# Performance work log

Measured on AMD Instinct MI355X. Metric: run time of the kernel, lower is better.

## Reference

```python
import jax, jax.numpy as jnp
import numpy as np

NUM_NODES = 100000
NODE_FEAT_DIM = 512
EDGE_FEAT_DIM = 512
MEM_DIM = NODE_FEAT_DIM + EDGE_FEAT_DIM  # 1024
BATCH = 65536


def setup_inputs() -> dict:
    key = jax.random.key(0)
    k_ids, k_mem, k_emb, kq, ks, kk = jax.random.split(key, 6)
    scale = 1.0 / np.sqrt(MEM_DIM)
    inp = {
        "node_ids": jax.random.randint(k_ids, (BATCH,), 0, NUM_NODES, dtype=jnp.int64)
        if jax.config.jax_enable_x64 else
        jax.random.randint(k_ids, (BATCH,), 0, NUM_NODES, dtype=jnp.int32),
        # memory bank: (N, 1, D); randomized (instead of the zero init) so math is non-trivial
        "node_memories": jax.random.normal(k_mem, (NUM_NODES, 1, MEM_DIM), dtype=jnp.float32) * 0.02,
        "node_embedding": jax.random.normal(k_emb, (NUM_NODES, MEM_DIM), dtype=jnp.float32) * 0.02,
        "Wq": jax.random.normal(jax.random.fold_in(kq, 0), (MEM_DIM, NODE_FEAT_DIM), dtype=jnp.float32) * scale,
        "bq": jnp.zeros((NODE_FEAT_DIM,), dtype=jnp.float32),
        "Ws": jax.random.normal(jax.random.fold_in(ks, 0), (MEM_DIM, NODE_FEAT_DIM), dtype=jnp.float32) * scale,
        "bs": jnp.zeros((NODE_FEAT_DIM,), dtype=jnp.float32),
        "Wk": jax.random.normal(jax.random.fold_in(kk, 0), (MEM_DIM, NODE_FEAT_DIM), dtype=jnp.float32) * scale,
        "bk": jnp.zeros((NODE_FEAT_DIM,), dtype=jnp.float32),
    }
    return inp


def reference(node_ids, node_memories, node_embedding, Wq, bq, Ws, bs, Wk, bk):
    ids = node_ids.astype(jnp.int32)
    # torch.sum(node_memories[ids], dim=2): reduces feature dim -> (B, 1)
    mem_sum = jnp.sum(node_memories[ids], axis=2)          # (B, 1)
    x = mem_sum + node_embedding[ids]                      # broadcast -> (B, D)
    q = jax.nn.sigmoid(x @ Wq + bq)                        # (B, node_feat_dim)
    s = jax.nn.sigmoid(x @ Ws + bs)
    k = jax.nn.sigmoid(x @ Wk + bk)
    return (q, s, k)
```

## Files before the change

kernel.cpp:

```cpp
#include <hip/hip_runtime.h>
#include <hip/hip_bf16.h>
#include <stdint.h>

#define BATCH_N 65536
#define KDIM 1024
#define NTOT 1536

typedef __bf16 bf16x8 __attribute__((ext_vector_type(8)));
typedef float f32x4 __attribute__((ext_vector_type(4)));

__device__ __forceinline__ unsigned short f2bf(float f) {
    unsigned u = __builtin_bit_cast(unsigned, f);
    u += 0x7FFFu + ((u >> 16) & 1u);
    return (unsigned short)(u >> 16);
}

__global__ __launch_bounds__(256) void prep_kernel(
    const int* __restrict__ ids,
    const float* __restrict__ mem,
    const float* __restrict__ emb,
    unsigned short* __restrict__ x)
{
    const int b    = blockIdx.x * 4 + (threadIdx.x >> 6);
    const int lane = threadIdx.x & 63;
    const int id   = ids[b];
    const float4* m4 = (const float4*)(mem + (size_t)id * KDIM) + lane;
    const float4* e4 = (const float4*)(emb + (size_t)id * KDIM) + lane;
    float4 v0 = m4[0];
    float4 v1 = m4[64];
    float4 v2 = m4[128];
    float4 v3 = m4[192];
    float s = (v0.x + v0.y + v0.z + v0.w) + (v1.x + v1.y + v1.z + v1.w)
            + (v2.x + v2.y + v2.z + v2.w) + (v3.x + v3.y + v3.z + v3.w);
    #pragma unroll
    for (int off = 1; off < 64; off <<= 1) s += __shfl_xor(s, off, 64);
    unsigned short* xb = x + (size_t)b * KDIM;
    #pragma unroll
    for (int q = 0; q < 4; ++q) {
        float4 e = e4[q * 64];
        ushort4 o;
        o.x = f2bf(s + e.x);
        o.y = f2bf(s + e.y);
        o.z = f2bf(s + e.z);
        o.w = f2bf(s + e.w);
        const int k   = q * 256 + lane * 4;
        const int ksw = k ^ ((b & 7) << 3);
        *(ushort4*)(xb + ksw) = o;
    }
}

__global__ __launch_bounds__(256) void wconv_kernel(
    const float* __restrict__ Wq, const float* __restrict__ Ws,
    const float* __restrict__ Wk, unsigned short* __restrict__ wt)
{
    const int gt = blockIdx.x * 256 + threadIdx.x;
    const int n  = gt % NTOT;
    const int kb = (gt / NTOT) * 4;
    const float* W = (n < 512) ? Wq : ((n < 1024) ? Ws : Wk);
    const int nn = n & 511;
    ushort4 o;
    o.x = f2bf(W[(size_t)(kb + 0) * 512 + nn]);
    o.y = f2bf(W[(size_t)(kb + 1) * 512 + nn]);
    o.z = f2bf(W[(size_t)(kb + 2) * 512 + nn]);
    o.w = f2bf(W[(size_t)(kb + 3) * 512 + nn]);
    const int ksw = kb ^ ((n & 7) << 3);
    *(ushort4*)(wt + (size_t)n * KDIM + ksw) = o;
}

#define BM 256
#define BN 256
#define BK 64
#define MT (BATCH_N / BM)
#define NT (NTOT / BN)
#define NWG (MT * NT)

#define BAR() asm volatile("s_barrier" ::: "memory")
#define VM4() asm volatile("s_waitcnt vmcnt(4)" ::: "memory")
#define VM0() asm volatile("s_waitcnt vmcnt(0)" ::: "memory")
#define AS1 __attribute__((address_space(1)))
#define AS3 __attribute__((address_space(3)))

__global__ __launch_bounds__(512, 2) void gemm_kernel(
    const unsigned short* __restrict__ X,
    const unsigned short* __restrict__ Wt,
    const float* __restrict__ bq, const float* __restrict__ bs,
    const float* __restrict__ bk, float* __restrict__ out)
{
    __shared__ __align__(16) unsigned short sA[32768];
    __shared__ __align__(16) unsigned short sB[32768];

    const int tid  = threadIdx.x;
    const int xcd  = blockIdx.x & 7;
    const int idx  = blockIdx.x >> 3;
    const int wgid = xcd * (NWG / 8) + idx;
    const int nt   = wgid % NT;
    const int mt   = wgid / NT;
    const int m0   = mt * BM;
    const int n0   = nt * BN;
    const int wid  = tid >> 6;
    const int lane = tid & 63;
    const int wm   = wid >> 2;
    const int wn   = wid & 3;
    const int r16  = lane & 15;
    const int kb0  = (lane >> 4) << 4;
    const int ksw  = (r16 & 7) << 4;

    f32x4 acc[8][4];
    #pragma unroll
    for (int i = 0; i < 8; i++)
        #pragma unroll
        for (int j = 0; j < 4; j++)
            acc[i][j] = f32x4{0.f, 0.f, 0.f, 0.f};

    bf16x8 af0[4][2], af1[4][2], bfr0[2][2], bfr1[2][2];

    const unsigned short* gA = X  + (size_t)(m0 + (tid >> 3)) * KDIM + (tid & 7) * 8;
    const unsigned short* gB = Wt + (size_t)(n0 + (tid >> 3)) * KDIM + (tid & 7) * 8;
    const int ldst = (tid & 448) * 8;

#define STG_A(slot, h, kt) do {                                                 \
    _Pragma("unroll")                                                            \
    for (int c = 0; c < 2; ++c)                                                  \
        __builtin_amdgcn_global_load_lds(                                        \
            (const AS1 void*)(gA + (size_t)((h) * 128 + c * 64) * KDIM + (kt) * BK), \
            (AS3 void*)(&sA[((slot) * 2 + (h)) * 8192 + c * 4096 + ldst]),       \
            16, 0, 0);                                                           \
} while (0)
#define STG_B(slot, h, kt) do {                                                 \
    _Pragma("unroll")                                                            \
    for (int c = 0; c < 2; ++c)                                                  \
        __builtin_amdgcn_global_load_lds(                                        \
            (const AS1 void*)(gB + (size_t)((h) * 128 + c * 64) * KDIM + (kt) * BK), \
            (AS3 void*)(&sB[((slot) * 2 + (h)) * 8192 + c * 4096 + ldst]),       \
            16, 0, 0);                                                           \
} while (0)

#define LDA(SET, slot, qa) do {                                                 \
    const char* p = (const char*)&sA[((slot) * 2 + (qa)) * 8192];                \
    _Pragma("unroll")                                                            \
    for (int i = 0; i < 4; ++i)                                                  \
        _Pragma("unroll")                                                        \
        for (int kk = 0; kk < 2; ++kk)                                           \
            SET[i][kk] = *(const bf16x8*)(p + (wm * 64 + i * 16 + r16) * 128     \
                                            + ((kk * 64 + kb0) ^ ksw));          \
} while (0)
#define LDB(SET, slot, qb) do {                                                 \
    const char* p = (const char*)&sB[((slot) * 2 + (qb)) * 8192];                \
    _Pragma("unroll")                                                            \
    for (int j = 0; j < 2; ++j)                                                  \
        _Pragma("unroll")                                                        \
        for (int kk = 0; kk < 2; ++kk)                                           \
            SET[j][kk] = *(const bf16x8*)(p + (wn * 32 + j * 16 + r16) * 128     \
                                            + ((kk * 64 + kb0) ^ ksw));          \
} while (0)

#define MM(QA, QB, ASET, BSET) do {                                             \
    __builtin_amdgcn_s_setprio(1);                                               \
    _Pragma("unroll")                                                            \
    for (int i = 0; i < 4; ++i)                                                  \
        _Pragma("unroll")                                                        \
        for (int j = 0; j < 2; ++j)                                              \
            _Pragma("unroll")                                                    \
            for (int kk = 0; kk < 2; ++kk)                                       \
                acc[(QA) * 4 + i][(QB) * 2 + j] =                                \
                    __builtin_amdgcn_mfma_f32_16x16x32_bf16(                     \
                        ASET[i][kk], BSET[j][kk],                                \
                        acc[(QA) * 4 + i][(QB) * 2 + j], 0, 0, 0);               \
    __builtin_amdgcn_s_setprio(0);                                               \
} while (0)

    STG_A(0, 0, 0); STG_A(0, 1, 0); STG_B(0, 0, 0); STG_B(0, 1, 0);
    STG_A(1, 0, 1); STG_B(1, 1, 1); STG_A(1, 1, 1);
    VM0();
    BAR();
    LDA(af0, 0, 0); LDB(bfr0, 0, 0);

    #pragma unroll 1
    for (int t = 0; t < 7; ++t) {
        const int ka = 2 * t + 1, kb2 = 2 * t + 2, kc = 2 * t + 3;
        MM(0, 0, af0, bfr0);
        LDB(bfr1, 0, 1); STG_B(1, 0, ka);                        BAR();
        MM(0, 1, af0, bfr1);
        LDA(af1, 0, 1); STG_A(0, 0, kb2);                        BAR();
        MM(1, 1, af1, bfr1); STG_B(0, 1, kb2); VM4();            BAR();
        MM(1, 0, af1, bfr0);
        LDA(af0, 1, 0); LDB(bfr0, 1, 0); STG_A(0, 1, kb2);       BAR();
        MM(0, 0, af0, bfr0);
        LDB(bfr1, 1, 1); STG_B(0, 0, kb2);                       BAR();
        MM(0, 1, af0, bfr1);
        LDA(af1, 1, 1); STG_A(1, 0, kc);                         BAR();
        MM(1, 1, af1, bfr1); STG_B(1, 1, kc); VM4();             BAR();
        MM(1, 0, af1, bfr0);
        LDA(af0, 0, 0); LDB(bfr0, 0, 0); STG_A(1, 1, kc);        BAR();
    }
    MM(0, 0, af0, bfr0);
    LDB(bfr1, 0, 1); STG_B(1, 0, 15);                            BAR();
    MM(0, 1, af0, bfr1); LDA(af1, 0, 1);                         BAR();
    MM(1, 1, af1, bfr1); VM0();                                  BAR();
    MM(1, 0, af1, bfr0); LDA(af0, 1, 0); LDB(bfr0, 1, 0);        BAR();
    MM(0, 0, af0, bfr0); LDB(bfr1, 1, 1);                        BAR();
    MM(0, 1, af0, bfr1); LDA(af1, 1, 1);                         BAR();
    MM(1, 1, af1, bfr1);                                         BAR();
    MM(1, 0, af1, bfr0);

    const int grp = nt >> 1;
    const float* bias = (grp == 0) ? bq : ((grp == 1) ? bs : bk);
    float* obase = out + (size_t)grp * ((size_t)BATCH_N * 512);
    const int cb = (nt & 1) * 256;
    #pragma unroll
    for (int qb = 0; qb < 2; ++qb)
        #pragma unroll
        for (int j = 0; j < 2; ++j) {
            const int col = cb + qb * 128 + wn * 32 + j * 16 + r16;
            const float bv = bias[col];
            #pragma unroll
            for (int qa = 0; qa < 2; ++qa)
                #pragma unroll
                for (int i = 0; i < 4; ++i) {
                    const int rbase = m0 + qa * 128 + wm * 64 + i * 16 + ((lane >> 4) << 2);
                    #pragma unroll
                    for (int r = 0; r < 4; ++r) {
                        float v = acc[qa * 4 + i][qb * 2 + j][r] + bv;
                        v = 1.0f / (1.0f + __expf(-v));
                        __builtin_nontemporal_store(v, &obase[(size_t)(rbase + r) * 512 + col]);
                    }
                }
        }
#undef STG_A
#undef STG_B
#undef LDA
#undef LDB
#undef MM
}

extern "C" void kernel_launch(void* const* d_in, const int* in_sizes, int n_in,
                              void* d_out, int out_size, void* d_ws, size_t ws_size,
                              hipStream_t stream) {
    const int*   ids = (const int*)d_in[0];
    const float* mem = (const float*)d_in[1];
    const float* emb = (const float*)d_in[2];
    const float* Wq  = (const float*)d_in[3];
    const float* bq  = (const float*)d_in[4];
    const float* Ws  = (const float*)d_in[5];
    const float* bs  = (const float*)d_in[6];
    const float* Wk  = (const float*)d_in[7];
    const float* bk  = (const float*)d_in[8];
    float* out = (float*)d_out;

    unsigned short* x  = (unsigned short*)d_ws;
    unsigned short* wt = x + (size_t)BATCH_N * KDIM;

    hipLaunchKernelGGL(wconv_kernel, dim3(NTOT), dim3(256), 0, stream, Wq, Ws, Wk, wt);
    hipLaunchKernelGGL(prep_kernel, dim3(BATCH_N / 4), dim3(256), 0, stream, ids, mem, emb, x);
    hipLaunchKernelGGL(gemm_kernel, dim3(NWG), dim3(512), 0, stream,
                       x, wt, bq, bs, bk, out);
}
```

Baseline: 394.6 us.

## Switch GEMM to FP8 MFMA and fold memory-sum term via weight column sums

```diff
diff --git a/kernel.cpp b/kernel.cpp
--- a/kernel.cpp
+++ b/kernel.cpp
@@ -6,88 +6,101 @@
 #define KDIM 1024
 #define NTOT 1536
 
-typedef __bf16 bf16x8 __attribute__((ext_vector_type(8)));
+typedef long long i64;
 typedef float f32x4 __attribute__((ext_vector_type(4)));
 
-__device__ __forceinline__ unsigned short f2bf(float f) {
-    unsigned u = __builtin_bit_cast(unsigned, f);
-    u += 0x7FFFu + ((u >> 16) & 1u);
-    return (unsigned short)(u >> 16);
+__device__ __forceinline__ unsigned pk4(float4 f, float s) {
+    int w = __builtin_amdgcn_cvt_pk_fp8_f32(f.x * s, f.y * s, 0, false);
+    w = __builtin_amdgcn_cvt_pk_fp8_f32(f.z * s, f.w * s, w, true);
+    return (unsigned)w;
 }
 
 __global__ __launch_bounds__(256) void prep_kernel(
     const int* __restrict__ ids,
     const float* __restrict__ mem,
     const float* __restrict__ emb,
-    unsigned short* __restrict__ x)
+    unsigned char* __restrict__ x,
+    float* __restrict__ rs)
 {
     const int b    = blockIdx.x * 4 + (threadIdx.x >> 6);
     const int lane = threadIdx.x & 63;
     const int id   = ids[b];
     const float4* m4 = (const float4*)(mem + (size_t)id * KDIM) + lane;
-    const float4* e4 = (const float4*)(emb + (size_t)id * KDIM) + lane;
-    float4 v0 = m4[0];
-    float4 v1 = m4[64];
-    float4 v2 = m4[128];
-    float4 v3 = m4[192];
+    float4 v0 = m4[0], v1 = m4[64], v2 = m4[128], v3 = m4[192];
     float s = (v0.x + v0.y + v0.z + v0.w) + (v1.x + v1.y + v1.z + v1.w)
             + (v2.x + v2.y + v2.z + v2.w) + (v3.x + v3.y + v3.z + v3.w);
     #pragma unroll
     for (int off = 1; off < 64; off <<= 1) s += __shfl_xor(s, off, 64);
-    unsigned short* xb = x + (size_t)b * KDIM;
-    #pragma unroll
-    for (int q = 0; q < 4; ++q) {
-        float4 e = e4[q * 64];
-        ushort4 o;
-        o.x = f2bf(s + e.x);
-        o.y = f2bf(s + e.y);
-        o.z = f2bf(s + e.z);
-        o.w = f2bf(s + e.w);
-        const int k   = q * 256 + lane * 4;
-        const int ksw = k ^ ((b & 7) << 3);
-        *(ushort4*)(xb + ksw) = o;
-    }
+    if (lane == 0) rs[b] = s;
+
+    const float4* e4 = (const float4*)(emb + (size_t)id * KDIM) + lane * 4;
+    float4 f0 = e4[0], f1 = e4[1], f2 = e4[2], f3 = e4[3];
+    const unsigned w0 = pk4(f0, 64.f), w1 = pk4(f1, 64.f);
+    const unsigned w2 = pk4(f2, 64.f), w3 = pk4(f3, 64.f);
+    uint4 val = (b & 1) ? uint4{w2, w3, w0, w1} : uint4{w0, w1, w2, w3};
+    const int dst = (lane * 16) ^ (((b >> 1) & 3) << 4);
+    *(uint4*)(x + (size_t)b * KDIM + dst) = val;
 }
 
 __global__ __launch_bounds__(256) void wconv_kernel(
     const float* __restrict__ Wq, const float* __restrict__ Ws,
-    const float* __restrict__ Wk, unsigned short* __restrict__ wt)
-{
-    const int gt = blockIdx.x * 256 + threadIdx.x;
-    const int n  = gt % NTOT;
-    const int kb = (gt / NTOT) * 4;
+    const float* __restrict__ Wk, unsigned char* __restrict__ wt)
+{
+    const int gt  = blockIdx.x * 256 + threadIdx.x;
+    const int n   = gt % NTOT;
+    const int kb4 = (gt / NTOT) * 4;
     const float* W = (n < 512) ? Wq : ((n < 1024) ? Ws : Wk);
     const int nn = n & 511;
-    ushort4 o;
-    o.x = f2bf(W[(size_t)(kb + 0) * 512 + nn]);
-    o.y = f2bf(W[(size_t)(kb + 1) * 512 + nn]);
-    o.z = f2bf(W[(size_t)(kb + 2) * 512 + nn]);
-    o.w = f2bf(W[(size_t)(kb + 3) * 512 + nn]);
-    const int ksw = kb ^ ((n & 7) << 3);
-    *(ushort4*)(wt + (size_t)n * KDIM + ksw) = o;
+    float4 f;
+    f.x = W[(size_t)(kb4 + 0) * 512 + nn];
+    f.y = W[(size_t)(kb4 + 1) * 512 + nn];
+    f.z = W[(size_t)(kb4 + 2) * 512 + nn];
+    f.w = W[(size_t)(kb4 + 3) * 512 + nn];
+    const unsigned w = pk4(f, 64.f);
+    const int dst = kb4 ^ ((n & 7) << 3);
+    *(unsigned*)(wt + (size_t)n * KDIM + dst) = w;
+}
+
+__global__ __launch_bounds__(256) void colsum_kernel(
+    const float* __restrict__ Wq, const float* __restrict__ Ws,
+    const float* __restrict__ Wk, float* __restrict__ csum)
+{
+    const int gt = blockIdx.x * 256 + threadIdx.x;
+    const float* W = (gt < 512) ? Wq : ((gt < 1024) ? Ws : Wk);
+    const int n = gt & 511;
+    float s0 = 0.f, s1 = 0.f, s2 = 0.f, s3 = 0.f;
+    #pragma unroll 4
+    for (int k = 0; k < 1024; k += 4) {
+        s0 += W[(size_t)(k + 0) * 512 + n];
+        s1 += W[(size_t)(k + 1) * 512 + n];
+        s2 += W[(size_t)(k + 2) * 512 + n];
+        s3 += W[(size_t)(k + 3) * 512 + n];
+    }
+    csum[gt] = (s0 + s1) + (s2 + s3);
 }
 
 #define BM 256
 #define BN 256
-#define BK 64
 #define MT (BATCH_N / BM)
 #define NT (NTOT / BN)
 #define NWG (MT * NT)
 
 #define BAR() asm volatile("s_barrier" ::: "memory")
-#define VM4() asm volatile("s_waitcnt vmcnt(4)" ::: "memory")
+#define VM2() asm volatile("s_waitcnt vmcnt(2)" ::: "memory")
 #define VM0() asm volatile("s_waitcnt vmcnt(0)" ::: "memory")
 #define AS1 __attribute__((address_space(1)))
 #define AS3 __attribute__((address_space(3)))
 
 __global__ __launch_bounds__(512, 2) void gemm_kernel(
-    const unsigned short* __restrict__ X,
-    const unsigned short* __restrict__ Wt,
+    const unsigned char* __restrict__ X,
+    const unsigned char* __restrict__ Wt,
+    const float* __restrict__ csum,
+    const float* __restrict__ rs,
     const float* __restrict__ bq, const float* __restrict__ bs,
     const float* __restrict__ bk, float* __restrict__ out)
 {
-    __shared__ __align__(16) unsigned short sA[32768];
-    __shared__ __align__(16) unsigned short sB[32768];
+    __shared__ __align__(16) unsigned char sA[32768];
+    __shared__ __align__(16) unsigned char sB[32768];
 
     const int tid  = threadIdx.x;
     const int xcd  = blockIdx.x & 7;
@@ -102,8 +115,8 @@
     const int wm   = wid >> 2;
     const int wn   = wid & 3;
     const int r16  = lane & 15;
-    const int kb0  = (lane >> 4) << 4;
-    const int ksw  = (r16 & 7) << 4;
+    const int kb0  = (lane >> 4) << 3;
+    const int ksw  = (r16 & 7) << 3;
 
     f32x4 acc[8][4];
     #pragma unroll
@@ -112,28 +125,20 @@
         for (int j = 0; j < 4; j++)
             acc[i][j] = f32x4{0.f, 0.f, 0.f, 0.f};
 
-    bf16x8 af0[4][2], af1[4][2], bfr0[2][2], bfr1[2][2];
-
-    const unsigned short* gA = X  + (size_t)(m0 + (tid >> 3)) * KDIM + (tid & 7) * 8;
-    const unsigned short* gB = Wt + (size_t)(n0 + (tid >> 3)) * KDIM + (tid & 7) * 8;
-    const int ldst = (tid & 448) * 8;
-
-#define STG_A(slot, h, kt) do {                                                 \
-    _Pragma("unroll")                                                            \
-    for (int c = 0; c < 2; ++c)                                                  \
-        __builtin_amdgcn_global_load_lds(                                        \
-            (const AS1 void*)(gA + (size_t)((h) * 128 + c * 64) * KDIM + (kt) * BK), \
-            (AS3 void*)(&sA[((slot) * 2 + (h)) * 8192 + c * 4096 + ldst]),       \
-            16, 0, 0);                                                           \
-} while (0)
-#define STG_B(slot, h, kt) do {                                                 \
-    _Pragma("unroll")                                                            \
-    for (int c = 0; c < 2; ++c)                                                  \
-        __builtin_amdgcn_global_load_lds(                                        \
-            (const AS1 void*)(gB + (size_t)((h) * 128 + c * 64) * KDIM + (kt) * BK), \
-            (AS3 void*)(&sB[((slot) * 2 + (h)) * 8192 + c * 4096 + ldst]),       \
-            16, 0, 0);                                                           \
-} while (0)
+    i64 af0[4][2], af1[4][2], bfr0[2][2], bfr1[2][2];
+
+    const unsigned char* gA = X  + (size_t)(m0 + (tid >> 2)) * KDIM + (tid & 3) * 16;
+    const unsigned char* gB = Wt + (size_t)(n0 + (tid >> 2)) * KDIM + (tid & 3) * 16;
+    const int ldst = tid * 16;
+
+#define STG_A(slot, h, kt) \
+    __builtin_amdgcn_global_load_lds( \
+        (const AS1 void*)(gA + (size_t)(h) * 128 * KDIM + (kt) * 64), \
+        (AS3 void*)(&sA[((slot) * 2 + (h)) * 8192 + ldst]), 16, 0, 0)
+#define STG_B(slot, h, kt) \
+    __builtin_amdgcn_global_load_lds( \
+        (const AS1 void*)(gB + (size_t)(h) * 128 * KDIM + (kt) * 64), \
+        (AS3 void*)(&sB[((slot) * 2 + (h)) * 8192 + ldst]), 16, 0, 0)
 
 #define LDA(SET, slot, qa) do {                                                 \
     const char* p = (const char*)&sA[((slot) * 2 + (qa)) * 8192];                \
@@ -141,8 +146,8 @@
     for (int i = 0; i < 4; ++i)                                                  \
         _Pragma("unroll")                                                        \
         for (int kk = 0; kk < 2; ++kk)                                           \
-            SET[i][kk] = *(const bf16x8*)(p + (wm * 64 + i * 16 + r16) * 128     \
-                                            + ((kk * 64 + kb0) ^ ksw));          \
+            SET[i][kk] = *(const i64*)(p + (wm * 64 + i * 16 + r16) * 64         \
+                                         + ((kk * 32 + kb0) ^ ksw));             \
 } while (0)
 #define LDB(SET, slot, qb) do {                                                 \
     const char* p = (const char*)&sB[((slot) * 2 + (qb)) * 8192];                \
@@ -150,8 +155,8 @@
     for (int j = 0; j < 2; ++j)                                                  \
         _Pragma("unroll")                                                        \
         for (int kk = 0; kk < 2; ++kk)                                           \
-            SET[j][kk] = *(const bf16x8*)(p + (wn * 32 + j * 16 + r16) * 128     \
-                                            + ((kk * 64 + kb0) ^ ksw));          \
+            SET[j][kk] = *(const i64*)(p + (wn * 32 + j * 16 + r16) * 64         \
+                                         + ((kk * 32 + kb0) ^ ksw));             \
 } while (0)
 
 #define MM(QA, QB, ASET, BSET) do {                                             \
@@ -163,7 +168,7 @@
             _Pragma("unroll")                                                    \
             for (int kk = 0; kk < 2; ++kk)                                       \
                 acc[(QA) * 4 + i][(QB) * 2 + j] =                                \
-                    __builtin_amdgcn_mfma_f32_16x16x32_bf16(                     \
+                    __builtin_amdgcn_mfma_f32_16x16x32_fp8_fp8(                  \
                         ASET[i][kk], BSET[j][kk],                                \
                         acc[(QA) * 4 + i][(QB) * 2 + j], 0, 0, 0);               \
     __builtin_amdgcn_s_setprio(0);                                               \
@@ -182,14 +187,14 @@
         LDB(bfr1, 0, 1); STG_B(1, 0, ka);                        BAR();
         MM(0, 1, af0, bfr1);
         LDA(af1, 0, 1); STG_A(0, 0, kb2);                        BAR();
-        MM(1, 1, af1, bfr1); STG_B(0, 1, kb2); VM4();            BAR();
+        MM(1, 1, af1, bfr1); STG_B(0, 1, kb2); VM2();            BAR();
         MM(1, 0, af1, bfr0);
         LDA(af0, 1, 0); LDB(bfr0, 1, 0); STG_A(0, 1, kb2);       BAR();
         MM(0, 0, af0, bfr0);
         LDB(bfr1, 1, 1); STG_B(0, 0, kb2);                       BAR();
         MM(0, 1, af0, bfr1);
         LDA(af1, 1, 1); STG_A(1, 0, kc);                         BAR();
-        MM(1, 1, af1, bfr1); STG_B(1, 1, kc); VM4();             BAR();
+        MM(1, 1, af1, bfr1); STG_B(1, 1, kc); VM2();             BAR();
         MM(1, 0, af1, bfr0);
         LDA(af0, 0, 0); LDB(bfr0, 0, 0); STG_A(1, 1, kc);        BAR();
     }
@@ -203,6 +208,7 @@
     MM(1, 1, af1, bfr1);                                         BAR();
     MM(1, 0, af1, bfr0);
 
+    const float inv = 1.0f / 4096.0f;
     const int grp = nt >> 1;
     const float* bias = (grp == 0) ? bq : ((grp == 1) ? bs : bk);
     float* obase = out + (size_t)grp * ((size_t)BATCH_N * 512);
@@ -211,18 +217,21 @@
     for (int qb = 0; qb < 2; ++qb)
         #pragma unroll
         for (int j = 0; j < 2; ++j) {
-            const int col = cb + qb * 128 + wn * 32 + j * 16 + r16;
-            const float bv = bias[col];
+            const int coll = cb + qb * 128 + wn * 32 + j * 16 + r16;
+            const float bv = bias[coll];
+            const float cv = csum[n0 + qb * 128 + wn * 32 + j * 16 + r16];
             #pragma unroll
             for (int qa = 0; qa < 2; ++qa)
                 #pragma unroll
                 for (int i = 0; i < 4; ++i) {
                     const int rbase = m0 + qa * 128 + wm * 64 + i * 16 + ((lane >> 4) << 2);
+                    const float4 rv = *(const float4*)(rs + rbase);
                     #pragma unroll
                     for (int r = 0; r < 4; ++r) {
-                        float v = acc[qa * 4 + i][qb * 2 + j][r] + bv;
+                        const float rsv = (r == 0) ? rv.x : (r == 1) ? rv.y : (r == 2) ? rv.z : rv.w;
+                        float v = acc[qa * 4 + i][qb * 2 + j][r] * inv + rsv * cv + bv;
                         v = 1.0f / (1.0f + __expf(-v));
-                        __builtin_nontemporal_store(v, &obase[(size_t)(rbase + r) * 512 + col]);
+                        __builtin_nontemporal_store(v, &obase[(size_t)(rbase + r) * 512 + coll]);
                     }
                 }
         }
@@ -247,11 +256,14 @@
     const float* bk  = (const float*)d_in[8];
     float* out = (float*)d_out;
 
-    unsigned short* x  = (unsigned short*)d_ws;
-    unsigned short* wt = x + (size_t)BATCH_N * KDIM;
+    unsigned char* x  = (unsigned char*)d_ws;
+    unsigned char* wt = x + (size_t)BATCH_N * KDIM;
+    float* csum = (float*)(wt + (size_t)NTOT * KDIM);
+    float* rs   = csum + NTOT;
 
     hipLaunchKernelGGL(wconv_kernel, dim3(NTOT), dim3(256), 0, stream, Wq, Ws, Wk, wt);
-    hipLaunchKernelGGL(prep_kernel, dim3(BATCH_N / 4), dim3(256), 0, stream, ids, mem, emb, x);
+    hipLaunchKernelGGL(colsum_kernel, dim3(6), dim3(256), 0, stream, Wq, Ws, Wk, csum);
+    hipLaunchKernelGGL(prep_kernel, dim3(BATCH_N / 4), dim3(256), 0, stream, ids, mem, emb, x, rs);
     hipLaunchKernelGGL(gemm_kernel, dim3(NWG), dim3(512), 0, stream,
-                       x, wt, bq, bs, bk, out);
-}
+                       x, wt, csum, rs, bq, bs, bk, out);
+}
```

New measurement: 394.3 us. Within noise of the previous version (-0.1%).
